# Performance work log

Hardware: AMD Instinct MI355X
Metric: run time of the kernel (lower is better)

## Reference

```python
import jax, jax.numpy as jnp
import numpy as np
from jax import lax

DIM = 128
EXP = 4
K = 7
B, D, H, W = 2, 48, 48, 48


def setup_inputs() -> dict:
    key = jax.random.key(0)
    ks = jax.random.split(key, 8)
    C, Ch = DIM, EXP * DIM
    x = jax.random.normal(ks[0], (B, C, D, H, W), dtype=jnp.float32)
    dw_w = jax.random.normal(ks[1], (C, 1, K, K, K), dtype=jnp.float32) * 0.05
    dw_b = jnp.zeros((C,), dtype=jnp.float32)
    ln_g = jnp.ones((C,), dtype=jnp.float32)
    ln_b = jnp.zeros((C,), dtype=jnp.float32)
    w1 = jax.random.normal(ks[2], (C, Ch), dtype=jnp.float32) * (1.0 / np.sqrt(C))
    b1 = jnp.zeros((Ch,), dtype=jnp.float32)
    grn_g = jnp.zeros((Ch,), dtype=jnp.float32)
    grn_b = jnp.zeros((Ch,), dtype=jnp.float32)
    w2 = jax.random.normal(ks[3], (Ch, C), dtype=jnp.float32) * (1.0 / np.sqrt(Ch))
    b2 = jnp.zeros((C,), dtype=jnp.float32)
    return {"x": x, "dw_w": dw_w, "dw_b": dw_b, "ln_g": ln_g, "ln_b": ln_b,
            "w1": w1, "b1": b1, "grn_g": grn_g, "grn_b": grn_b, "w2": w2, "b2": b2}


def reference(x, dw_w, dw_b, ln_g, ln_b, w1, b1, grn_g, grn_b, w2, b2):
    C = x.shape[1]
    pad = (K - 1) // 2
    # depthwise 3D conv, NCDHW
    y = lax.conv_general_dilated(
        x, dw_w, window_strides=(1, 1, 1),
        padding=[(pad, pad)] * 3,
        feature_group_count=C,
        dimension_numbers=("NCDHW", "OIDHW", "NCDHW"))
    y = y + dw_b[None, :, None, None, None]
    y = jnp.transpose(y, (0, 2, 3, 4, 1))  # [B,D,H,W,C] channels-last
    # LayerNorm over channels (eps=1e-6)
    mu = jnp.mean(y, axis=-1, keepdims=True)
    var = jnp.mean((y - mu) ** 2, axis=-1, keepdims=True)
    y = (y - mu) / jnp.sqrt(var + 1e-6) * ln_g + ln_b
    # pwconv1 + GELU (exact)
    h = jax.nn.gelu(jnp.einsum("bdhwc,ce->bdhwe", y, w1) + b1, approximate=False)
    # GRN: global L2 over spatial dims per channel, divisive norm over channel mean
    gx = jnp.sqrt(jnp.sum(h * h, axis=(1, 2, 3), keepdims=True))  # [B,1,1,1,Ch]
    nx = gx / (jnp.mean(gx, axis=-1, keepdims=True) + 1e-6)
    h = grn_g * (h * nx) + grn_b + h
    # pwconv2
    y = jnp.einsum("bdhwe,ec->bdhwc", h, w2) + b2
    y = jnp.transpose(y, (0, 4, 1, 2, 3))  # back to NCDHW
    return x + y
```

## Files before the change

### kernel.cpp

```cpp
#include <hip/hip_runtime.h>
#include <math.h>

#define PVOX 110592
#define CDIM 128
#define EDIM 512

typedef __attribute__((ext_vector_type(8))) short short8_t;
typedef __attribute__((ext_vector_type(4))) float float4_t;

__device__ __forceinline__ unsigned short f2bf(float f) {
  unsigned int u = __float_as_uint(f);
  unsigned int r = (u + 0x7FFFu + ((u >> 16) & 1u)) >> 16;
  return (unsigned short)r;
}
__device__ __forceinline__ float bf2f(unsigned short s) {
  return __uint_as_float(((unsigned int)s) << 16);
}
__device__ __forceinline__ int swz(int row, int col) {
  return (row << 7) + ((((col >> 3) ^ (row & 15)) << 3) | (col & 7));
}
__device__ __forceinline__ int swzO(int c, int p) {
  return (c << 7) + (p ^ ((c & 15) << 2));
}

__global__ __launch_bounds__(256) void k0_wprep(
    const float* __restrict__ w1, const float* __restrict__ w2,
    unsigned short* __restrict__ w1t, unsigned short* __restrict__ w2t) {
  int idx = blockIdx.x * 256 + threadIdx.x;
  int e = idx >> 7, c = idx & 127;
  w1t[e * 128 + c] = f2bf(w1[c * 512 + e]);
  w2t[c * 512 + e] = f2bf(w2[e * 128 + c]);
}

__global__ __launch_bounds__(384) void k1_dwconv(
    const float* __restrict__ x, const float* __restrict__ dw_w,
    const float* __restrict__ dw_b, float* __restrict__ yconv) {
  __shared__ float sx[22 * 14 * 60];
  int bx = blockIdx.x;
  int ht = bx % 6;  int tmp = bx / 6;
  int dtile = tmp % 3; tmp /= 3;
  int c = tmp & 127; int b = tmp >> 7;
  int d0 = dtile * 16, h0 = ht * 8;
  const float* xp = x + (size_t)(b * 128 + c) * PVOX;
  int t = threadIdx.x;
  for (int i = t; i < 4312; i += 384) {
    int gi = i % 14; int rr = i / 14; int hh = rr % 14; int r = rr / 14;
    int gd = d0 - 3 + r, gh = h0 - 3 + hh;
    float4_t v = {0.f, 0.f, 0.f, 0.f};
    if ((unsigned)gd < 48u && (unsigned)gh < 48u && gi >= 1 && gi <= 12)
      v = *(const float4_t*)&xp[(gd * 48 + gh) * 48 + gi * 4 - 4];
    *(float4_t*)&sx[r * 840 + hh * 60 + gi * 4] = v;
  }
  __syncthreads();
  int wc = t % 6; int h = (t / 6) % 8; int dt = t / 48;
  int w0 = wc * 8;
  const float* wbase = dw_w + c * 343;
  float bias = dw_b[c];
  float a0[8], a1[8];
#pragma unroll
  for (int i = 0; i < 8; i++) { a0[i] = bias; a1[i] = bias; }
  for (int kh = 0; kh < 7; kh++) {
    int hl = h + kh;
    const float* hp = &sx[hl * 60 + w0];
#pragma unroll
    for (int r8 = 0; r8 < 8; r8++) {
      int r = 2 * dt + r8;
      const float* rp = &hp[r * 840];
      float4_t v4[4];
#pragma unroll
      for (int g = 0; g < 4; g++) v4[g] = *(const float4_t*)&rp[g * 4];
      if (r8 <= 6) {
        const float* wr = wbase + r8 * 49 + kh * 7;
#pragma unroll
        for (int kw = 0; kw < 7; kw++) {
          float wv = wr[kw];
#pragma unroll
          for (int wi = 0; wi < 8; wi++) {
            int vi = wi + kw + 1;
            a0[wi] += wv * v4[vi >> 2][vi & 3];
          }
        }
      }
      if (r8 >= 1) {
        const float* wr = wbase + (r8 - 1) * 49 + kh * 7;
#pragma unroll
        for (int kw = 0; kw < 7; kw++) {
          float wv = wr[kw];
#pragma unroll
          for (int wi = 0; wi < 8; wi++) {
            int vi = wi + kw + 1;
            a1[wi] += wv * v4[vi >> 2][vi & 3];
          }
        }
      }
    }
  }
  int dg = d0 + 2 * dt;
  float* op0 = yconv + (size_t)(b * 128 + c) * PVOX + ((size_t)dg * 48 + (h0 + h)) * 48 + w0;
  float* op1 = op0 + 48 * 48;
  float4_t o;
  o[0] = a0[0]; o[1] = a0[1]; o[2] = a0[2]; o[3] = a0[3]; *(float4_t*)&op0[0] = o;
  o[0] = a0[4]; o[1] = a0[5]; o[2] = a0[6]; o[3] = a0[7]; *(float4_t*)&op0[4] = o;
  o[0] = a1[0]; o[1] = a1[1]; o[2] = a1[2]; o[3] = a1[3]; *(float4_t*)&op1[0] = o;
  o[0] = a1[4]; o[1] = a1[5]; o[2] = a1[6]; o[3] = a1[7]; *(float4_t*)&op1[4] = o;
}

__global__ __launch_bounds__(256) void k2_ln(
    const float* __restrict__ yconv, const float* __restrict__ ln_g,
    const float* __restrict__ ln_b, unsigned short* __restrict__ ycl) {
  __shared__ float sy[128 * 65];
  __shared__ float smean[64], srstd[64];
  int bx = blockIdx.x;
  int b = bx / 1728;
  int p0 = (bx % 1728) * 64;
  int t = threadIdx.x;
  int v = t & 63, c4 = t >> 6;
  const float* yp = yconv + (size_t)b * 128 * PVOX + p0;
  for (int cc = 0; cc < 32; cc++) {
    int c = cc * 4 + c4;
    sy[c * 65 + v] = yp[(size_t)c * PVOX + v];
  }
  __syncthreads();
  if (t < 64) {
    float s = 0.f, ss = 0.f;
    for (int c = 0; c < 128; c++) { float val = sy[c * 65 + t]; s += val; ss += val * val; }
    float mu = s * (1.f / 128.f);
    float var = ss * (1.f / 128.f) - mu * mu;
    smean[t] = mu; srstd[t] = rsqrtf(var + 1e-6f);
  }
  __syncthreads();
  unsigned short* op = ycl + ((size_t)b * PVOX + p0) * 128;
  for (int it = 0; it < 32; it++) {
    int idx = it * 256 + t;
    int vv = idx >> 7, c = idx & 127;
    float val = (sy[c * 65 + vv] - smean[vv]) * srstd[vv] * ln_g[c] + ln_b[c];
    op[vv * 128 + c] = f2bf(val);
  }
}

__global__ __launch_bounds__(256) void k3_pw1(
    const unsigned short* __restrict__ ycl, const unsigned short* __restrict__ w1t,
    const float* __restrict__ b1, unsigned short* __restrict__ h,
    float* __restrict__ gsum) {
  __shared__ short smem[2 * 128 * 128];
  short* sA = smem;
  short* sB = smem + 128 * 128;
  int bx = blockIdx.x;
  int et = bx & 3; int pt = bx >> 2;
  int e0 = et << 7;
  int b = (pt >= 864) ? 1 : 0;
  int t = threadIdx.x;
  for (int it = 0; it < 8; it++) {
    int flat = it * 2048 + t * 8;
    int row = flat >> 7, col = flat & 127;
    *(uint4*)&sA[swz(row, col)] = *(const uint4*)&ycl[((size_t)(pt * 128 + row)) * 128 + col];
    *(uint4*)&sB[swz(row, col)] = *(const uint4*)&w1t[(e0 + row) * 128 + col];
  }
  __syncthreads();
  int wave = t >> 6, lane = t & 63;
  int wm = (wave >> 1) * 64, wn = (wave & 1) * 64;
  int ln15 = lane & 15, q = lane >> 4;
  float4_t acc[4][4] = {};
  for (int kk = 0; kk < 4; kk++) {
    int k0 = kk * 32 + q * 8;
    short8_t af[4], bf[4];
#pragma unroll
    for (int i = 0; i < 4; i++)
      af[i] = *(const short8_t*)&sA[swz(wm + i * 16 + ln15, k0)];
#pragma unroll
    for (int j = 0; j < 4; j++)
      bf[j] = *(const short8_t*)&sB[swz(wn + j * 16 + ln15, k0)];
#pragma unroll
    for (int i = 0; i < 4; i++)
#pragma unroll
      for (int j = 0; j < 4; j++)
        acc[i][j] = __builtin_amdgcn_mfma_f32_16x16x32_bf16(af[i], bf[j], acc[i][j], 0, 0, 0);
  }
  __syncthreads();
  float biasv[4];
#pragma unroll
  for (int j = 0; j < 4; j++) biasv[j] = b1[e0 + wn + j * 16 + ln15];
  float ssq[4] = {0.f, 0.f, 0.f, 0.f};
#pragma unroll
  for (int i = 0; i < 4; i++) {
#pragma unroll
    for (int j = 0; j < 4; j++) {
      int e_local = wn + j * 16 + ln15;
#pragma unroll
      for (int r = 0; r < 4; r++) {
        float val = acc[i][j][r] + biasv[j];
        float g = 0.5f * val * (1.0f + erff(val * 0.70710678118f));
        ssq[j] += g * g;
        sA[swz(wm + i * 16 + q * 4 + r, e_local)] = (short)f2bf(g);
      }
    }
  }
#pragma unroll
  for (int j = 0; j < 4; j++) {
    ssq[j] += __shfl_xor(ssq[j], 16);
    ssq[j] += __shfl_xor(ssq[j], 32);
  }
  if (q == 0) {
#pragma unroll
    for (int j = 0; j < 4; j++)
      atomicAdd(&gsum[b * 512 + e0 + wn + j * 16 + ln15], ssq[j]);
  }
  __syncthreads();
  for (int it = 0; it < 8; it++) {
    int flat = it * 2048 + t * 8;
    int row = flat >> 7, col = flat & 127;
    *(uint4*)&h[((size_t)(pt * 128 + row)) * 512 + e0 + col] = *(const uint4*)&sA[swz(row, col)];
  }
}

__global__ __launch_bounds__(512) void k4_grn(
    const float* __restrict__ gsum, const float* __restrict__ grn_g,
    const float* __restrict__ grn_b, const float* __restrict__ w2,
    const float* __restrict__ b2, float* __restrict__ s, float* __restrict__ badd) {
  __shared__ float red[512];
  int t = threadIdx.x;
  for (int b = 0; b < 2; b++) {
    float gx = sqrtf(gsum[b * 512 + t]);
    red[t] = gx;
    __syncthreads();
    for (int off = 256; off > 0; off >>= 1) {
      if (t < off) red[t] += red[t + off];
      __syncthreads();
    }
    float mean = red[0] * (1.f / 512.f);
    __syncthreads();
    s[b * 512 + t] = 1.0f + grn_g[t] * (gx / (mean + 1e-6f));
  }
  if (t < 128) {
    float acc = b2[t];
    for (int e = 0; e < 512; e++) acc += grn_b[e] * w2[e * 128 + t];
    badd[t] = acc;
  }
}

__global__ __launch_bounds__(256) void k5_pw2(
    const unsigned short* __restrict__ h, const unsigned short* __restrict__ w2t,
    const float* __restrict__ s, const float* __restrict__ badd,
    const float* __restrict__ x, float* __restrict__ out) {
  __shared__ short smem[2 * 128 * 128];
  short* sA = smem;
  short* sB = smem + 128 * 128;
  int bx = blockIdx.x;
  int b = bx / 864;
  int p0 = (bx % 864) * 128;
  int vp0 = bx * 128;
  int t = threadIdx.x;
  int wave = t >> 6, lane = t & 63;
  int wm = (wave >> 1) * 64, wn = (wave & 1) * 64;
  int ln15 = lane & 15, q = lane >> 4;
  const float* sb = s + b * 512;
  float4_t acc[4][4] = {};
  for (int ec = 0; ec < 4; ec++) {
    int e0 = ec * 128;
    for (int it = 0; it < 8; it++) {
      int flat = it * 2048 + t * 8;
      int row = flat >> 7, col = flat & 127;
      uint4 raw = *(const uint4*)&h[((size_t)(vp0 + row)) * 512 + e0 + col];
      const unsigned short* us = (const unsigned short*)&raw;
      unsigned short ov[8];
#pragma unroll
      for (int i2 = 0; i2 < 8; i2++)
        ov[i2] = f2bf(bf2f(us[i2]) * sb[e0 + col + i2]);
      *(uint4*)&sA[swz(row, col)] = *(const uint4*)ov;
      *(uint4*)&sB[swz(row, col)] = *(const uint4*)&w2t[row * 512 + e0 + col];
    }
    __syncthreads();
    for (int kk = 0; kk < 4; kk++) {
      int k0 = kk * 32 + q * 8;
      short8_t af[4], bf[4];
#pragma unroll
      for (int i = 0; i < 4; i++)
        af[i] = *(const short8_t*)&sA[swz(wm + i * 16 + ln15, k0)];
#pragma unroll
      for (int j = 0; j < 4; j++)
        bf[j] = *(const short8_t*)&sB[swz(wn + j * 16 + ln15, k0)];
#pragma unroll
      for (int i = 0; i < 4; i++)
#pragma unroll
        for (int j = 0; j < 4; j++)
          acc[i][j] = __builtin_amdgcn_mfma_f32_16x16x32_bf16(af[i], bf[j], acc[i][j], 0, 0, 0);
    }
    __syncthreads();
  }
  float* sO = (float*)smem;
#pragma unroll
  for (int i = 0; i < 4; i++)
#pragma unroll
    for (int j = 0; j < 4; j++) {
      int c = wn + j * 16 + ln15;
#pragma unroll
      for (int r = 0; r < 4; r++)
        sO[swzO(c, wm + i * 16 + q * 4 + r)] = acc[i][j][r];
    }
  __syncthreads();
  for (int it = 0; it < 16; it++) {
    int flat4 = it * 256 + t;
    int c = flat4 >> 5, col4 = (flat4 & 31) * 4;
    float4_t v = *(const float4_t*)&sO[swzO(c, col4)];
    float bd = badd[c];
    size_t gi = (size_t)(b * 128 + c) * PVOX + p0 + col4;
    float4_t xv = *(const float4_t*)&x[gi];
    v[0] += bd + xv[0]; v[1] += bd + xv[1]; v[2] += bd + xv[2]; v[3] += bd + xv[3];
    *(float4_t*)&out[gi] = v;
  }
}

extern "C" void kernel_launch(void* const* d_in, const int* in_sizes, int n_in,
                              void* d_out, int out_size, void* d_ws, size_t ws_size,
                              hipStream_t stream) {
  (void)in_sizes; (void)n_in; (void)out_size; (void)ws_size;
  const float* x    = (const float*)d_in[0];
  const float* dw_w = (const float*)d_in[1];
  const float* dw_b = (const float*)d_in[2];
  const float* ln_g = (const float*)d_in[3];
  const float* ln_b = (const float*)d_in[4];
  const float* w1   = (const float*)d_in[5];
  const float* b1   = (const float*)d_in[6];
  const float* grn_g= (const float*)d_in[7];
  const float* grn_b= (const float*)d_in[8];
  const float* w2   = (const float*)d_in[9];
  const float* b2   = (const float*)d_in[10];
  float* outp = (float*)d_out;

  char* w = (char*)d_ws;
  float*          yconv = (float*)(w);
  unsigned short* ycl   = (unsigned short*)(w + 113246208);
  unsigned short* h     = (unsigned short*)(w + 169869312);
  float*          gsum  = (float*)(w + 396361728);
  float*          s     = (float*)(w + 396365824);
  float*          badd  = (float*)(w + 396369920);
  unsigned short* w1t   = (unsigned short*)(w + 396370432);
  unsigned short* w2t   = (unsigned short*)(w + 396501504);

  hipMemsetAsync(gsum, 0, 2 * 512 * sizeof(float), stream);
  k0_wprep<<<256, 256, 0, stream>>>(w1, w2, w1t, w2t);
  k1_dwconv<<<4608, 384, 0, stream>>>(x, dw_w, dw_b, yconv);
  k2_ln<<<3456, 256, 0, stream>>>(yconv, ln_g, ln_b, ycl);
  k3_pw1<<<6912, 256, 0, stream>>>(ycl, w1t, b1, h, gsum);
  k4_grn<<<1, 512, 0, stream>>>(gsum, grn_g, grn_b, w2, b2, s, badd);
  k5_pw2<<<1728, 256, 0, stream>>>(h, w2t, s, badd, x, outp);
}
```

Before: 1.023 ms.

## Restructure depthwise conv as streaming depth sweep with rolling accumulators

The depthwise 3D conv now has each block sweep half the depth of one channel. It keeps a double-buffered single D-plane in shared memory and a rolling window of 7 output-plane accumulators in registers. This removes the halo reloading of 22x14 tiles and makes each input plane load once per half-depth. The cost is a grid shrink from 4608 to 512 blocks of 576 threads, a barrier per plane, and reduced parallelism that may underfill the GPU.

```diff
diff --git a/kernel.cpp b/kernel.cpp
--- a/kernel.cpp
+++ b/kernel.cpp
@@ -32,77 +32,86 @@
   w2t[c * 512 + e] = f2bf(w2[e * 128 + c]);
 }
 
-__global__ __launch_bounds__(384) void k1_dwconv(
+__global__ __launch_bounds__(576, 4) void k1_dwconv(
     const float* __restrict__ x, const float* __restrict__ dw_w,
     const float* __restrict__ dw_b, float* __restrict__ yconv) {
-  __shared__ float sx[22 * 14 * 60];
+  __shared__ float sx[2][54 * 60];
   int bx = blockIdx.x;
-  int ht = bx % 6;  int tmp = bx / 6;
-  int dtile = tmp % 3; tmp /= 3;
-  int c = tmp & 127; int b = tmp >> 7;
-  int d0 = dtile * 16, h0 = ht * 8;
+  int dh = bx & 1;
+  int c = (bx >> 1) & 127;
+  int b = bx >> 8;
+  int d0 = dh * 24;
   const float* xp = x + (size_t)(b * 128 + c) * PVOX;
-  int t = threadIdx.x;
-  for (int i = t; i < 4312; i += 384) {
-    int gi = i % 14; int rr = i / 14; int hh = rr % 14; int r = rr / 14;
-    int gd = d0 - 3 + r, gh = h0 - 3 + hh;
-    float4_t v = {0.f, 0.f, 0.f, 0.f};
-    if ((unsigned)gd < 48u && (unsigned)gh < 48u && gi >= 1 && gi <= 12)
-      v = *(const float4_t*)&xp[(gd * 48 + gh) * 48 + gi * 4 - 4];
-    *(float4_t*)&sx[r * 840 + hh * 60 + gi * 4] = v;
-  }
-  __syncthreads();
-  int wc = t % 6; int h = (t / 6) % 8; int dt = t / 48;
-  int w0 = wc * 8;
+  float* yp = yconv + (size_t)(b * 128 + c) * PVOX;
   const float* wbase = dw_w + c * 343;
   float bias = dw_b[c];
-  float a0[8], a1[8];
-#pragma unroll
-  for (int i = 0; i < 8; i++) { a0[i] = bias; a1[i] = bias; }
-  for (int kh = 0; kh < 7; kh++) {
-    int hl = h + kh;
-    const float* hp = &sx[hl * 60 + w0];
-#pragma unroll
-    for (int r8 = 0; r8 < 8; r8++) {
-      int r = 2 * dt + r8;
-      const float* rp = &hp[r * 840];
-      float4_t v4[4];
-#pragma unroll
-      for (int g = 0; g < 4; g++) v4[g] = *(const float4_t*)&rp[g * 4];
-      if (r8 <= 6) {
-        const float* wr = wbase + r8 * 49 + kh * 7;
-#pragma unroll
-        for (int kw = 0; kw < 7; kw++) {
-          float wv = wr[kw];
-#pragma unroll
-          for (int wi = 0; wi < 8; wi++) {
-            int vi = wi + kw + 1;
-            a0[wi] += wv * v4[vi >> 2][vi & 3];
+  int t = threadIdx.x;
+  int h = t / 12, wc = t % 12;
+  int w0 = wc * 4;
+  for (int i = t; i < 2 * 54 * 60; i += 576) ((float*)sx)[i] = 0.f;
+  __syncthreads();
+  {
+    int p = d0 - 3;
+    if (p >= 0) {
+      float4_t v = *(const float4_t*)&xp[((size_t)p * 48 + h) * 48 + w0];
+      *(float4_t*)&sx[0][(h + 3) * 60 + 4 + w0] = v;
+    }
+  }
+  float acc[7][4];
+#pragma unroll
+  for (int j = 0; j < 7; j++)
+#pragma unroll
+    for (int i = 0; i < 4; i++) acc[j][i] = bias;
+  __syncthreads();
+
+  for (int q = 0; q < 30; ++q) {
+    int p = d0 - 3 + q;
+    int pn = p + 1;
+    bool ldok = (pn >= 0) && (pn <= 47) && (pn <= d0 + 26);
+    float4_t stg = {0.f, 0.f, 0.f, 0.f};
+    if (ldok) stg = *(const float4_t*)&xp[((size_t)pn * 48 + h) * 48 + w0];
+
+    const float* bufr = sx[q & 1];
+    if (p >= 0 && p <= 47) {
+#pragma unroll
+      for (int kh = 0; kh < 7; kh++) {
+        const float* rp = &bufr[(h + kh) * 60 + w0];
+        float4_t v0 = *(const float4_t*)&rp[0];
+        float4_t v1 = *(const float4_t*)&rp[4];
+        float4_t v2 = *(const float4_t*)&rp[8];
+        float v[12] = {v0[0], v0[1], v0[2], v0[3], v1[0], v1[1], v1[2], v1[3],
+                       v2[0], v2[1], v2[2], v2[3]};
+#pragma unroll
+        for (int kd = 0; kd < 7; kd++) {
+          if ((unsigned)(q - kd) < 24u) {
+            const float* wr = wbase + kd * 49 + kh * 7;
+#pragma unroll
+            for (int kw = 0; kw < 7; kw++) {
+              float wv = wr[kw];
+#pragma unroll
+              for (int wi = 0; wi < 4; wi++)
+                acc[6 - kd][wi] += wv * v[wi + kw + 1];
+            }
           }
         }
       }
-      if (r8 >= 1) {
-        const float* wr = wbase + (r8 - 1) * 49 + kh * 7;
-#pragma unroll
-        for (int kw = 0; kw < 7; kw++) {
-          float wv = wr[kw];
-#pragma unroll
-          for (int wi = 0; wi < 8; wi++) {
-            int vi = wi + kw + 1;
-            a1[wi] += wv * v4[vi >> 2][vi & 3];
-          }
-        }
-      }
-    }
-  }
-  int dg = d0 + 2 * dt;
-  float* op0 = yconv + (size_t)(b * 128 + c) * PVOX + ((size_t)dg * 48 + (h0 + h)) * 48 + w0;
-  float* op1 = op0 + 48 * 48;
-  float4_t o;
-  o[0] = a0[0]; o[1] = a0[1]; o[2] = a0[2]; o[3] = a0[3]; *(float4_t*)&op0[0] = o;
-  o[0] = a0[4]; o[1] = a0[5]; o[2] = a0[6]; o[3] = a0[7]; *(float4_t*)&op0[4] = o;
-  o[0] = a1[0]; o[1] = a1[1]; o[2] = a1[2]; o[3] = a1[3]; *(float4_t*)&op1[0] = o;
-  o[0] = a1[4]; o[1] = a1[5]; o[2] = a1[6]; o[3] = a1[7]; *(float4_t*)&op1[4] = o;
+    }
+    if (q >= 6) {
+      int d = d0 + q - 6;
+      float4_t o;
+      o[0] = acc[0][0]; o[1] = acc[0][1]; o[2] = acc[0][2]; o[3] = acc[0][3];
+      *(float4_t*)&yp[((size_t)d * 48 + h) * 48 + w0] = o;
+    }
+#pragma unroll
+    for (int j = 0; j < 6; j++)
+#pragma unroll
+      for (int i = 0; i < 4; i++) acc[j][i] = acc[j + 1][i];
+#pragma unroll
+    for (int i = 0; i < 4; i++) acc[6][i] = bias;
+    float* bufw = (float*)sx[(q + 1) & 1];
+    *(float4_t*)&bufw[(h + 3) * 60 + 4 + w0] = stg;
+    __syncthreads();
+  }
 }
 
 __global__ __launch_bounds__(256) void k2_ln(
@@ -339,7 +348,7 @@
 
   hipMemsetAsync(gsum, 0, 2 * 512 * sizeof(float), stream);
   k0_wprep<<<256, 256, 0, stream>>>(w1, w2, w1t, w2t);
-  k1_dwconv<<<4608, 384, 0, stream>>>(x, dw_w, dw_b, yconv);
+  k1_dwconv<<<512, 576, 0, stream>>>(x, dw_w, dw_b, yconv);
   k2_ln<<<3456, 256, 0, stream>>>(yconv, ln_g, ln_b, ycl);
   k3_pw1<<<6912, 256, 0, stream>>>(ycl, w1t, b1, h, gsum);
   k4_grn<<<1, 512, 0, stream>>>(gsum, grn_g, grn_b, w2, b2, s, badd);
```

Result: faster. 996.1 us (-2.6%).
